# Optimization experiments

Hardware: AMD Instinct MI355X
Metric: run time of the kernel (lower is better)

Reference implementation:

```python
import jax, jax.numpy as jnp
import numpy as np

B, S, D = 4, 512, 2048      # batch, seq, hidden
DFF = 5632                   # SwiGLU intermediate
E, TOPK, R = 8, 2, 16        # experts, top-k, lora rank
SCALE = 32.0 / 16.0          # lora alpha / r


def setup_inputs() -> dict:
    key = jax.random.key(0)
    ks = jax.random.split(key, 18)
    rn = lambda k, shape, s=0.02: (jax.random.normal(k, shape, dtype=jnp.float32) * s)
    return {
        "data": jax.random.normal(ks[0], (B, S, D), dtype=jnp.float32),
        # shared base SwiGLU MLP (gate/up/down projections)
        "W1": rn(ks[1], (DFF, D)),
        "W3": rn(ks[2], (DFF, D)),
        "W2": rn(ks[3], (D, DFF)),
        # MixLoRA MoE adapter: router gate + per-expert LoRA on w1/w3/w2
        "gate_W": rn(ks[4], (E, D)),
        "A1": rn(ks[5], (E, R, D)), "B1": rn(ks[6], (E, DFF, R)),
        "A3": rn(ks[7], (E, R, D)), "B3": rn(ks[8], (E, DFF, R)),
        "A2": rn(ks[9], (E, R, DFF)), "B2": rn(ks[10], (E, D, R)),
        # plain LoRA adapter (second batch segment, _lora_forward path)
        "la1": rn(ks[11], (R, D)), "lb1": rn(ks[12], (DFF, R)),
        "la3": rn(ks[13], (R, D)), "lb3": rn(ks[14], (DFF, R)),
        "la2": rn(ks[15], (R, DFF)), "lb2": rn(ks[16], (D, R)),
    }


def reference(data, W1, W3, W2, gate_W, A1, B1, A3, B3, A2, B2,
              la1, lb1, la3, lb3, la2, lb2):
    half = B // 2

    # ---- segment 0: MixLoRA MoE adapter ----
    x = data[:half].reshape(-1, D)                      # [N, D] tokens
    N = x.shape[0]
    logits = x @ gate_W.T                               # [N, E] router logits
    probs = jax.nn.softmax(logits, axis=-1)
    topw, topi = jax.lax.top_k(probs, TOPK)
    topw = topw / jnp.sum(topw, axis=-1, keepdims=True)
    # dense routing weights (zero for non-selected experts)
    wd = jnp.zeros((N, E), x.dtype).at[jnp.arange(N)[:, None], topi].set(topw)

    bg = x @ W1.T                                       # [N, DFF] base gate proj
    bu = x @ W3.T                                       # [N, DFF] base up proj
    dg = jnp.einsum('enr,efr->enf', jnp.einsum('nd,erd->enr', x, A1), B1)
    du = jnp.einsum('enr,efr->enf', jnp.einsum('nd,erd->enr', x, A3), B3)
    h = jax.nn.silu(bg[None] + SCALE * dg) * (bu[None] + SCALE * du)  # [E,N,DFF]
    oe = jnp.einsum('enf,df->end', h, W2) \
        + SCALE * jnp.einsum('enr,edr->end', jnp.einsum('enf,erf->enr', h, A2), B2)
    moe_out = jnp.einsum('ne,end->nd', wd, oe).reshape(half, S, D)

    # ---- segment 1: plain LoRA adapter (_lora_forward) ----
    x2 = data[half:]                                    # [half, S, D]
    g2 = jax.nn.silu(x2 @ W1.T + SCALE * ((x2 @ la1.T) @ lb1.T))
    u2 = x2 @ W3.T + SCALE * ((x2 @ la3.T) @ lb3.T)
    h2 = g2 * u2
    out2 = h2 @ W2.T + SCALE * ((h2 @ la2.T) @ lb2.T)

    # index_copy over contiguous per-segment ranges == concat along dim 0
    final = jnp.concatenate([moe_out, out2], axis=0)    # [B, S, D]
    return final, logits
```

## Files before the change

kernel.cpp:

```cpp
#include <hip/hip_runtime.h>
#include <hip/hip_bf16.h>

#define DEVI __device__ __forceinline__

typedef __attribute__((ext_vector_type(8))) short short8;
typedef __attribute__((ext_vector_type(4))) float f32x4;

constexpr int D    = 2048;
constexpr int DFF  = 5632;
constexpr int NTOK = 2048;
constexpr int NMOE = 1024;
constexpr float KSCALE = 2.0f;

constexpr int NW      = 11648;
constexpr int COL_A1  = 11264;
constexpr int COL_A3  = 11392;
constexpr int COL_LA1 = 11520;
constexpr int COL_LA3 = 11536;

DEVI float bf2f(unsigned short u) { return __uint_as_float(((unsigned)u) << 16); }
DEVI unsigned short f2bf(float f) {
  unsigned u = __float_as_uint(f);
  u += 0x7FFFu + ((u >> 16) & 1u);
  return (unsigned short)(u >> 16);
}
DEVI float silu(float x) { return x / (1.f + __expf(-x)); }

struct CastSegs {
  const float* src[14];
  unsigned short* dst[14];
  int blk_end[14];
};

__global__ __launch_bounds__(256) void cast_segs_kernel(CastSegs cs) {
  int b = blockIdx.x;
  int s = 0;
  #pragma unroll
  for (int i = 0; i < 14; ++i) if (b >= cs.blk_end[i]) s = i + 1;
  int bstart = (s == 0) ? 0 : cs.blk_end[s - 1];
  size_t idx = ((size_t)(b - bstart) * 256 + threadIdx.x) * 4;
  float4 v = *(const float4*)(cs.src[s] + idx);
  ushort4 o;
  o.x = f2bf(v.x); o.y = f2bf(v.y); o.z = f2bf(v.z); o.w = f2bf(v.w);
  *(ushort4*)(cs.dst[s] + idx) = o;
}

__global__ __launch_bounds__(256) void transpose_ra_kernel(const float* __restrict__ A2,
                                                           const float* __restrict__ la2,
                                                           unsigned short* __restrict__ A2tb,
                                                           unsigned short* __restrict__ la2tb) {
  int f = blockIdx.x * 256 + threadIdx.x;
  int e = blockIdx.y;
  const float* src = (e < 8) ? (A2 + (size_t)e * 16 * DFF) : la2;
  unsigned short* dst = (e < 8) ? (A2tb + (size_t)e * DFF * 16) : la2tb;
  unsigned short tmp[16];
  #pragma unroll
  for (int r = 0; r < 16; ++r) tmp[r] = f2bf(src[(size_t)r * DFF + f]);
  #pragma unroll
  for (int r = 0; r < 16; ++r) dst[(size_t)f * 16 + r] = tmp[r];
}

__global__ __launch_bounds__(256) void gate_kernel(const float* __restrict__ x,
                                                   const float* __restrict__ gW,
                                                   float* __restrict__ logits_out,
                                                   int* __restrict__ gidx,
                                                   float* __restrict__ gwt) {
  int t = blockIdx.x * 4 + (threadIdx.x >> 6);
  int lane = threadIdx.x & 63;
  const float* xr = x + (size_t)t * D;
  float acc[8];
  #pragma unroll
  for (int e = 0; e < 8; ++e) acc[e] = 0.f;
  for (int k = lane; k < D; k += 64) {
    float xv = xr[k];
    #pragma unroll
    for (int e = 0; e < 8; ++e) acc[e] = fmaf(xv, gW[e * D + k], acc[e]);
  }
  #pragma unroll
  for (int e = 0; e < 8; ++e) {
    float v = acc[e];
    #pragma unroll
    for (int s = 32; s > 0; s >>= 1) v += __shfl_xor(v, s);
    acc[e] = v;
  }
  if (lane == 0) {
    #pragma unroll
    for (int e = 0; e < 8; ++e) logits_out[(size_t)t * 8 + e] = acc[e];
    int i1 = 0;
    #pragma unroll
    for (int e = 1; e < 8; ++e) if (acc[e] > acc[i1]) i1 = e;
    int i2 = (i1 == 0) ? 1 : 0;
    #pragma unroll
    for (int e = 0; e < 8; ++e) if (e != i1 && acc[e] > acc[i2]) i2 = e;
    float w1 = 1.f / (1.f + expf(acc[i2] - acc[i1]));
    gidx[t * 2] = i1; gidx[t * 2 + 1] = i2;
    gwt[t * 2] = w1;  gwt[t * 2 + 1] = 1.f - w1;
  }
}

typedef const void __attribute__((address_space(1)))* gp1_t;
typedef void __attribute__((address_space(3)))* lp3_t;
DEVI void gload_lds16(const void* g, void* l) {
  __builtin_amdgcn_global_load_lds((gp1_t)g, (lp3_t)l, 16, 0, 0);
}
#define S_BARRIER() asm volatile("s_barrier" ::: "memory")
#define LGKM0() do { asm volatile("s_waitcnt lgkmcnt(0)" ::: "memory"); \
                     __builtin_amdgcn_sched_barrier(0); } while (0)

template <int N> DEVI void vmcnt_() {
  static_assert(N == 0 || N == 4, "enumerate literals");
  if constexpr (N == 0)  asm volatile("s_waitcnt vmcnt(0)" ::: "memory");
  if constexpr (N == 4)  asm volatile("s_waitcnt vmcnt(4)" ::: "memory");
}

template <int BM, int BN, int WM, int WN, int MINW, int EPI>
__global__ __launch_bounds__(WM * WN * 64, MINW) void gemmP(
    const unsigned short* __restrict__ A,
    const unsigned short* __restrict__ B,
    int K,
    float* __restrict__ Cf,
    unsigned short* __restrict__ Cb,
    const float* __restrict__ addv,
    int ldc, int nbx) {
  constexpr int THREADS = WM * WN * 64;
  constexpr int RW = BM / WM;
  constexpr int CW = BN / WN;
  static_assert(RW == 64 && CW == 64, "template assumes 64x64 per-wave tile");
  constexpr int ATILE = BM * 128;
  constexpr int BTILE = BN * 128;
  constexpr int SLOT = ATILE + BTILE;
  constexpr int APARTS = BM * 8 / THREADS;
  constexpr int BPARTS = BN * 8 / THREADS;
  constexpr int BH = BPARTS / 2;

  __shared__ __align__(16) char smem[2 * SLOT];

  const int tid = threadIdx.x;
  const int wave = tid >> 6, lane = tid & 63;
  const int wm = wave / WN, wn = wave % WN;
  const int r15 = lane & 15, g = lane >> 4;

  const int nwg = (int)gridDim.x;
  const int bid = (int)blockIdx.x;
  const int wgid = (bid & 7) * (nwg >> 3) + (bid >> 3);
  const int bx = wgid % nbx, by = wgid / nbx;

  const unsigned short* Ablk = A + (size_t)by * BM * K;
  const unsigned short* Bblk = B + (size_t)bx * BN * K;

  int sgoA[APARTS], sgoB[BPARTS];
  #pragma unroll
  for (int j = 0; j < APARTS; ++j) {
    int tt = j * THREADS + tid;
    int row = tt >> 3;
    sgoA[j] = row * K + (((tt & 7) ^ (row & 7)) << 3);
  }
  #pragma unroll
  for (int j = 0; j < BPARTS; ++j) {
    int tt = j * THREADS + tid;
    int row = tt >> 3;
    sgoB[j] = row * K + (((tt & 7) ^ (row & 7)) << 3);
  }
  auto stageA = [&](int p, int k0) {
    char* s = smem + p * SLOT;
    #pragma unroll
    for (int j = 0; j < APARTS; ++j)
      gload_lds16((const char*)Ablk + ((size_t)(sgoA[j] + k0) << 1),
                  s + j * (THREADS * 16) + wave * 1024);
  };
  auto stageBh = [&](int p, int k0, int h) {
    char* s = smem + p * SLOT + ATILE;
    #pragma unroll
    for (int j = 0; j < BH; ++j)
      gload_lds16((const char*)Bblk + ((size_t)(sgoB[h * BH + j] + k0) << 1),
                  s + (h * BH + j) * (THREADS * 16) + wave * 1024);
  };

  const int arow0 = (wm * RW + r15) * 128;
  const int brow0 = (wn * CW + r15) * 128;
  const int s0 = ((g ^ (r15 & 7)) << 4);
  const int s1 = (((4 + g) ^ (r15 & 7)) << 4);

  f32x4 acc[4][4];
  #pragma unroll
  for (int m = 0; m < 4; ++m)
    #pragma unroll
    for (int n = 0; n < 4; ++n)
      #pragma unroll
      for (int j = 0; j < 4; ++j) acc[m][n][j] = 0.f;

  const int NT = K >> 6;

  stageA(0, 0);
  stageBh(0, 0, 0);
  stageBh(0, 0, 1);

  for (int t = 0; t < NT; ++t) {
    const int p = t & 1;
    const bool hn = (t + 1) < NT;
    const int k0n = (t + 1) << 6;
    if (hn) {
      stageA(p ^ 1, k0n);
      vmcnt_<4>();
    } else {
      vmcnt_<0>();
    }
    S_BARRIER();

    const char* sA = smem + p * SLOT;
    const char* sB = sA + ATILE;

    short8 bq[4][2], af[2][2];
    #pragma unroll
    for (int n = 0; n < 4; ++n) {
      bq[n][0] = *(const short8*)(sB + brow0 + n * 2048 + s0);
      bq[n][1] = *(const short8*)(sB + brow0 + n * 2048 + s1);
    }
    #pragma unroll
    for (int i = 0; i < 2; ++i) {
      af[i][0] = *(const short8*)(sA + arow0 + i * 2048 + s0);
      af[i][1] = *(const short8*)(sA + arow0 + i * 2048 + s1);
    }
    if (hn) stageBh(p ^ 1, k0n, 0);
    S_BARRIER();
    LGKM0();
    __builtin_amdgcn_s_setprio(1);
    #pragma unroll
    for (int i = 0; i < 2; ++i)
      #pragma unroll
      for (int n = 0; n < 4; ++n)
        #pragma unroll
        for (int kk = 0; kk < 2; ++kk)
          acc[i][n] = __builtin_amdgcn_mfma_f32_16x16x32_bf16(
              af[i][kk], bq[n][kk], acc[i][n], 0, 0, 0);
    __builtin_amdgcn_s_setprio(0);

    short8 ag[2][2];
    #pragma unroll
    for (int i = 0; i < 2; ++i) {
      ag[i][0] = *(const short8*)(sA + arow0 + (2 + i) * 2048 + s0);
      ag[i][1] = *(const short8*)(sA + arow0 + (2 + i) * 2048 + s1);
    }
    if (hn) stageBh(p ^ 1, k0n, 1);
    S_BARRIER();
    LGKM0();
    __builtin_amdgcn_s_setprio(1);
    #pragma unroll
    for (int i = 0; i < 2; ++i)
      #pragma unroll
      for (int n = 0; n < 4; ++n)
        #pragma unroll
        for (int kk = 0; kk < 2; ++kk)
          acc[2 + i][n] = __builtin_amdgcn_mfma_f32_16x16x32_bf16(
              ag[i][kk], bq[n][kk], acc[2 + i][n], 0, 0, 0);
    __builtin_amdgcn_s_setprio(0);

    S_BARRIER();
  }

  const int row0 = by * BM + wm * RW + (g << 2);
  const int col0 = bx * BN + wn * CW + r15;
  #pragma unroll
  for (int m = 0; m < 4; ++m) {
    #pragma unroll
    for (int n = 0; n < 4; ++n) {
      int col = col0 + n * 16;
      #pragma unroll
      for (int j = 0; j < 4; ++j) {
        int row = row0 + m * 16 + j;
        size_t off = (size_t)row * ldc + col;
        float v = acc[m][n][j];
        if (EPI == 1) Cb[off] = f2bf(v);
        else          Cf[off] = v + addv[off];
      }
    }
  }
}

DEVI float dot16bf(const float* a, const unsigned short* w) {
  short8 w0 = *(const short8*)w;
  short8 w1 = *(const short8*)(w + 8);
  float s = 0.f;
  #pragma unroll
  for (int i = 0; i < 8; ++i) s = fmaf(a[i],     bf2f((unsigned short)w0[i]), s);
  #pragma unroll
  for (int i = 0; i < 8; ++i) s = fmaf(a[8 + i], bf2f((unsigned short)w1[i]), s);
  return s;
}

__global__ __launch_bounds__(256) void h_kernel(
    const unsigned short* __restrict__ GU,
    const unsigned short* __restrict__ B1b,
    const unsigned short* __restrict__ B3b,
    const unsigned short* __restrict__ A2tb,
    const unsigned short* __restrict__ lb1b,
    const unsigned short* __restrict__ lb3b,
    const unsigned short* __restrict__ la2tb,
    const int* __restrict__ gidx, const float* __restrict__ gwt,
    unsigned short* __restrict__ Hb,
    float* __restrict__ qw) {
  const int t = blockIdx.x;
  const int tid = threadIdx.x;
  const unsigned short* gu = GU + (size_t)t * NW;
  unsigned short* hrow = Hb + (size_t)t * DFF;
  float qacc[32];
  #pragma unroll
  for (int r = 0; r < 32; ++r) qacc[r] = 0.f;
  float w1 = 0.f, w2 = 0.f;

  if (t < NMOE) {
    const int e1 = gidx[t * 2], e2 = gidx[t * 2 + 1];
    w1 = gwt[t * 2]; w2 = gwt[t * 2 + 1];
    float xa1a[16], xa1b[16], xa3a[16], xa3b[16];
    #pragma unroll
    for (int r = 0; r < 16; ++r) {
      xa1a[r] = bf2f(gu[COL_A1 + e1 * 16 + r]);
      xa1b[r] = bf2f(gu[COL_A1 + e2 * 16 + r]);
      xa3a[r] = bf2f(gu[COL_A3 + e1 * 16 + r]);
      xa3b[r] = bf2f(gu[COL_A3 + e2 * 16 + r]);
    }
    const unsigned short* B1e1 = B1b + (size_t)e1 * DFF * 16;
    const unsigned short* B1e2 = B1b + (size_t)e2 * DFF * 16;
    const unsigned short* B3e1 = B3b + (size_t)e1 * DFF * 16;
    const unsigned short* B3e2 = B3b + (size_t)e2 * DFF * 16;
    const unsigned short* A2e1 = A2tb + (size_t)e1 * DFF * 16;
    const unsigned short* A2e2 = A2tb + (size_t)e2 * DFF * 16;
    for (int i = 0; i < 22; ++i) {
      int f = tid + i * 256;
      float bg = bf2f(gu[f]), bu = bf2f(gu[DFF + f]);
      float dg1 = dot16bf(xa1a, B1e1 + f * 16);
      float du1 = dot16bf(xa3a, B3e1 + f * 16);
      float dg2 = dot16bf(xa1b, B1e2 + f * 16);
      float du2 = dot16bf(xa3b, B3e2 + f * 16);
      float h1 = silu(bg + KSCALE * dg1) * (bu + KSCALE * du1);
      float h2 = silu(bg + KSCALE * dg2) * (bu + KSCALE * du2);
      hrow[f] = f2bf(w1 * h1 + w2 * h2);
      short8 a0 = *(const short8*)(A2e1 + f * 16);
      short8 a1 = *(const short8*)(A2e1 + f * 16 + 8);
      short8 b0 = *(const short8*)(A2e2 + f * 16);
      short8 b1 = *(const short8*)(A2e2 + f * 16 + 8);
      #pragma unroll
      for (int r = 0; r < 8; ++r) {
        qacc[r]      = fmaf(h1, bf2f((unsigned short)a0[r]), qacc[r]);
        qacc[8 + r]  = fmaf(h1, bf2f((unsigned short)a1[r]), qacc[8 + r]);
        qacc[16 + r] = fmaf(h2, bf2f((unsigned short)b0[r]), qacc[16 + r]);
        qacc[24 + r] = fmaf(h2, bf2f((unsigned short)b1[r]), qacc[24 + r]);
      }
    }
  } else {
    float s1[16], s3[16];
    #pragma unroll
    for (int r = 0; r < 16; ++r) {
      s1[r] = bf2f(gu[COL_LA1 + r]);
      s3[r] = bf2f(gu[COL_LA3 + r]);
    }
    for (int i = 0; i < 22; ++i) {
      int f = tid + i * 256;
      float bg = bf2f(gu[f]), bu = bf2f(gu[DFF + f]);
      float dg = dot16bf(s1, lb1b + f * 16);
      float du = dot16bf(s3, lb3b + f * 16);
      float h = silu(bg + KSCALE * dg) * (bu + KSCALE * du);
      hrow[f] = f2bf(h);
      short8 a0 = *(const short8*)(la2tb + f * 16);
      short8 a1 = *(const short8*)(la2tb + f * 16 + 8);
      #pragma unroll
      for (int r = 0; r < 8; ++r) {
        qacc[r]     = fmaf(h, bf2f((unsigned short)a0[r]), qacc[r]);
        qacc[8 + r] = fmaf(h, bf2f((unsigned short)a1[r]), qacc[8 + r]);
      }
    }
  }

  #pragma unroll
  for (int r = 0; r < 32; ++r) {
    float v = qacc[r];
    #pragma unroll
    for (int s = 32; s > 0; s >>= 1) v += __shfl_xor(v, s);
    qacc[r] = v;
  }
  __shared__ float red[4][32];
  const int wave = tid >> 6, lane = tid & 63;
  if (lane == 0) {
    #pragma unroll
    for (int r = 0; r < 32; ++r) red[wave][r] = qacc[r];
  }
  __syncthreads();
  if (tid < 32) {
    float v = red[0][tid] + red[1][tid] + red[2][tid] + red[3][tid];
    float sc = (t < NMOE) ? ((tid < 16) ? (KSCALE * w1) : (KSCALE * w2)) : KSCALE;
    qw[(size_t)t * 32 + tid] = v * sc;
  }
}

__global__ __launch_bounds__(256) void ylora_kernel(const float* __restrict__ qw,
                                                    const unsigned short* __restrict__ B2b,
                                                    const unsigned short* __restrict__ lb2b,
                                                    const int* __restrict__ gidx,
                                                    float* __restrict__ ylora) {
  const int t = blockIdx.x;
  const int tid = threadIdx.x;
  const float* qr = qw + (size_t)t * 32;
  float q1[16], q2[16];
  #pragma unroll
  for (int r = 0; r < 16; ++r) { q1[r] = qr[r]; q2[r] = qr[16 + r]; }
  if (t < NMOE) {
    const unsigned short* p1 = B2b + (size_t)gidx[t * 2] * D * 16;
    const unsigned short* p2 = B2b + (size_t)gidx[t * 2 + 1] * D * 16;
    #pragma unroll
    for (int i = 0; i < 8; ++i) {
      int d = tid + i * 256;
      ylora[(size_t)t * D + d] = dot16bf(q1, p1 + d * 16) + dot16bf(q2, p2 + d * 16);
    }
  } else {
    #pragma unroll
    for (int i = 0; i < 8; ++i) {
      int d = tid + i * 256;
      ylora[(size_t)t * D + d] = dot16bf(q1, lb2b + d * 16);
    }
  }
}

extern "C" void kernel_launch(void* const* d_in, const int* in_sizes, int n_in,
                              void* d_out, int out_size, void* d_ws, size_t ws_size,
                              hipStream_t stream) {
  (void)in_sizes; (void)n_in; (void)out_size; (void)ws_size;
  const float* data = (const float*)d_in[0];
  const float* W1   = (const float*)d_in[1];
  const float* W3   = (const float*)d_in[2];
  const float* W2   = (const float*)d_in[3];
  const float* gW   = (const float*)d_in[4];
  const float* A1   = (const float*)d_in[5];
  const float* B1   = (const float*)d_in[6];
  const float* A3   = (const float*)d_in[7];
  const float* B3   = (const float*)d_in[8];
  const float* A2   = (const float*)d_in[9];
  const float* B2   = (const float*)d_in[10];
  const float* la1  = (const float*)d_in[11];
  const float* lb1  = (const float*)d_in[12];
  const float* la3  = (const float*)d_in[13];
  const float* lb3  = (const float*)d_in[14];
  const float* la2  = (const float*)d_in[15];
  const float* lb2  = (const float*)d_in[16];

  char* w = (char*)d_ws;
  size_t off = 0;
  auto alloc = [&](size_t bytes) -> char* {
    char* p = w + off;
    off += (bytes + 255) & ~(size_t)255;
    return p;
  };
  unsigned short* xb    = (unsigned short*)alloc((size_t)NTOK * D * 2);
  unsigned short* W13b  = (unsigned short*)alloc((size_t)NW * D * 2);
  unsigned short* W2b   = (unsigned short*)alloc((size_t)D * DFF * 2);
  unsigned short* B1b   = (unsigned short*)alloc((size_t)8 * DFF * 16 * 2);
  unsigned short* B3b   = (unsigned short*)alloc((size_t)8 * DFF * 16 * 2);
  unsigned short* A2tb  = (unsigned short*)alloc((size_t)8 * DFF * 16 * 2);
  unsigned short* la2tb = (unsigned short*)alloc((size_t)DFF * 16 * 2);
  unsigned short* lb1b  = (unsigned short*)alloc((size_t)DFF * 16 * 2);
  unsigned short* lb3b  = (unsigned short*)alloc((size_t)DFF * 16 * 2);
  unsigned short* lb2b  = (unsigned short*)alloc((size_t)D * 16 * 2);
  unsigned short* B2b   = (unsigned short*)alloc((size_t)8 * D * 16 * 2);
  int*   gidx = (int*)alloc((size_t)NMOE * 2 * 4);
  float* gwt  = (float*)alloc((size_t)NMOE * 2 * 4);
  unsigned short* GU    = (unsigned short*)alloc((size_t)NTOK * NW * 2);

  unsigned short* Hb = W13b;
  float* ylora = (float*)((char*)W13b + (size_t)NTOK * DFF * 2);
  float* qw    = (float*)xb;

  CastSegs cs;
  const float* srcs[14] = {data, W1, W3, W2, A1, A3, la1, la3, B1, B3, lb1, lb3, lb2, B2};
  unsigned short* dsts[14] = {
      xb, W13b, W13b + (size_t)DFF * D, W2b,
      W13b + (size_t)COL_A1 * D, W13b + (size_t)COL_A3 * D,
      W13b + (size_t)COL_LA1 * D, W13b + (size_t)COL_LA3 * D,
      B1b, B3b, lb1b, lb3b, lb2b, B2b};
  int ns[14] = {NTOK * D, DFF * D, DFF * D, DFF * D, 128 * D, 128 * D, 16 * D, 16 * D,
                8 * DFF * 16, 8 * DFF * 16, DFF * 16, DFF * 16, D * 16, 8 * D * 16};
  int total_blocks = 0;
  for (int i = 0; i < 14; ++i) {
    cs.src[i] = srcs[i];
    cs.dst[i] = dsts[i];
    total_blocks += ns[i] / 1024;
    cs.blk_end[i] = total_blocks;
  }
  cast_segs_kernel<<<total_blocks, 256, 0, stream>>>(cs);
  transpose_ra_kernel<<<dim3(DFF / 256, 9), 256, 0, stream>>>(A2, la2, A2tb, la2tb);
  hipMemsetAsync(W13b + (size_t)11552 * D, 0, (size_t)(NW - 11552) * D * 2, stream);

  gate_kernel<<<NMOE / 4, 256, 0, stream>>>(data, gW,
      (float*)d_out + (size_t)NTOK * D, gidx, gwt);

  gemmP<256, 128, 4, 2, 2, 1><<<(NTOK / 256) * (NW / 128), 512, 0, stream>>>(
      xb, W13b, D, (float*)nullptr, GU, (const float*)nullptr, NW, NW / 128);

  h_kernel<<<NTOK, 256, 0, stream>>>(GU, B1b, B3b, A2tb, lb1b, lb3b, la2tb,
                                     gidx, gwt, Hb, qw);

  ylora_kernel<<<NTOK, 256, 0, stream>>>(qw, B2b, lb2b, gidx, ylora);

  gemmP<128, 128, 2, 2, 2, 2><<<(NTOK / 128) * (D / 128), 256, 0, stream>>>(
      Hb, W2b, DFF, (float*)d_out, (unsigned short*)nullptr, ylora, D, D / 128);
}
```

Measured before the change: 358.1 us.

## Simplify GEMM pipeline to single-stage prefetch and shrink gate/up tile

The split-phase GEMM schedule is removed. It used to stage B in two halves between partial MFMA blocks, with extra barriers, lgkmcnt waits and setprio hints. Now each K-tile loads A and B in one prefetch, waits with vmcnt(8), reads all fragments, then runs the full 4x4 MFMA block. The gate/up projection GEMM also moves from 256x128 tiles with 8 waves to 128x128 tiles with 4 waves, doubling the grid. The aim is fewer barriers and better occupancy or load balance, at the cost of less interleaving of loads with compute and more redundant B-tile traffic.

```diff
diff --git a/kernel.cpp b/kernel.cpp
--- a/kernel.cpp
+++ b/kernel.cpp
@@ -104,17 +104,15 @@
   __builtin_amdgcn_global_load_lds((gp1_t)g, (lp3_t)l, 16, 0, 0);
 }
 #define S_BARRIER() asm volatile("s_barrier" ::: "memory")
-#define LGKM0() do { asm volatile("s_waitcnt lgkmcnt(0)" ::: "memory"); \
-                     __builtin_amdgcn_sched_barrier(0); } while (0)
 
 template <int N> DEVI void vmcnt_() {
-  static_assert(N == 0 || N == 4, "enumerate literals");
-  if constexpr (N == 0)  asm volatile("s_waitcnt vmcnt(0)" ::: "memory");
-  if constexpr (N == 4)  asm volatile("s_waitcnt vmcnt(4)" ::: "memory");
+  static_assert(N == 0 || N == 8, "enumerate literals");
+  if constexpr (N == 0) asm volatile("s_waitcnt vmcnt(0)" ::: "memory");
+  if constexpr (N == 8) asm volatile("s_waitcnt vmcnt(8)" ::: "memory");
 }
 
 template <int BM, int BN, int WM, int WN, int MINW, int EPI>
-__global__ __launch_bounds__(WM * WN * 64, MINW) void gemmP(
+__global__ __launch_bounds__(WM * WN * 64, MINW) void gemmM(
     const unsigned short* __restrict__ A,
     const unsigned short* __restrict__ B,
     int K,
@@ -131,7 +129,7 @@
   constexpr int SLOT = ATILE + BTILE;
   constexpr int APARTS = BM * 8 / THREADS;
   constexpr int BPARTS = BN * 8 / THREADS;
-  constexpr int BH = BPARTS / 2;
+  static_assert(APARTS + BPARTS == 8, "vmcnt gate literal assumes 8 loads/tile");
 
   __shared__ __align__(16) char smem[2 * SLOT];
 
@@ -161,19 +159,16 @@
     int row = tt >> 3;
     sgoB[j] = row * K + (((tt & 7) ^ (row & 7)) << 3);
   }
-  auto stageA = [&](int p, int k0) {
+  auto stage = [&](int p, int k0) {
     char* s = smem + p * SLOT;
     #pragma unroll
     for (int j = 0; j < APARTS; ++j)
       gload_lds16((const char*)Ablk + ((size_t)(sgoA[j] + k0) << 1),
                   s + j * (THREADS * 16) + wave * 1024);
-  };
-  auto stageBh = [&](int p, int k0, int h) {
-    char* s = smem + p * SLOT + ATILE;
-    #pragma unroll
-    for (int j = 0; j < BH; ++j)
-      gload_lds16((const char*)Bblk + ((size_t)(sgoB[h * BH + j] + k0) << 1),
-                  s + (h * BH + j) * (THREADS * 16) + wave * 1024);
+    #pragma unroll
+    for (int j = 0; j < BPARTS; ++j)
+      gload_lds16((const char*)Bblk + ((size_t)(sgoB[j] + k0) << 1),
+                  s + ATILE + j * (THREADS * 16) + wave * 1024);
   };
 
   const int arow0 = (wm * RW + r15) * 128;
@@ -191,17 +186,13 @@
 
   const int NT = K >> 6;
 
-  stageA(0, 0);
-  stageBh(0, 0, 0);
-  stageBh(0, 0, 1);
+  stage(0, 0);
 
   for (int t = 0; t < NT; ++t) {
     const int p = t & 1;
-    const bool hn = (t + 1) < NT;
-    const int k0n = (t + 1) << 6;
-    if (hn) {
-      stageA(p ^ 1, k0n);
-      vmcnt_<4>();
+    if (t + 1 < NT) {
+      stage(p ^ 1, (t + 1) << 6);
+      vmcnt_<8>();
     } else {
       vmcnt_<0>();
     }
@@ -210,50 +201,25 @@
     const char* sA = smem + p * SLOT;
     const char* sB = sA + ATILE;
 
-    short8 bq[4][2], af[2][2];
+    short8 bq[4][2], av[4][2];
     #pragma unroll
     for (int n = 0; n < 4; ++n) {
       bq[n][0] = *(const short8*)(sB + brow0 + n * 2048 + s0);
       bq[n][1] = *(const short8*)(sB + brow0 + n * 2048 + s1);
     }
     #pragma unroll
-    for (int i = 0; i < 2; ++i) {
-      af[i][0] = *(const short8*)(sA + arow0 + i * 2048 + s0);
-      af[i][1] = *(const short8*)(sA + arow0 + i * 2048 + s1);
-    }
-    if (hn) stageBh(p ^ 1, k0n, 0);
-    S_BARRIER();
-    LGKM0();
-    __builtin_amdgcn_s_setprio(1);
-    #pragma unroll
-    for (int i = 0; i < 2; ++i)
+    for (int m = 0; m < 4; ++m) {
+      av[m][0] = *(const short8*)(sA + arow0 + m * 2048 + s0);
+      av[m][1] = *(const short8*)(sA + arow0 + m * 2048 + s1);
+    }
+    #pragma unroll
+    for (int m = 0; m < 4; ++m)
       #pragma unroll
       for (int n = 0; n < 4; ++n)
         #pragma unroll
         for (int kk = 0; kk < 2; ++kk)
-          acc[i][n] = __builtin_amdgcn_mfma_f32_16x16x32_bf16(
-              af[i][kk], bq[n][kk], acc[i][n], 0, 0, 0);
-    __builtin_amdgcn_s_setprio(0);
-
-    short8 ag[2][2];
-    #pragma unroll
-    for (int i = 0; i < 2; ++i) {
-      ag[i][0] = *(const short8*)(sA + arow0 + (2 + i) * 2048 + s0);
-      ag[i][1] = *(const short8*)(sA + arow0 + (2 + i) * 2048 + s1);
-    }
-    if (hn) stageBh(p ^ 1, k0n, 1);
-    S_BARRIER();
-    LGKM0();
-    __builtin_amdgcn_s_setprio(1);
-    #pragma unroll
-    for (int i = 0; i < 2; ++i)
-      #pragma unroll
-      for (int n = 0; n < 4; ++n)
-        #pragma unroll
-        for (int kk = 0; kk < 2; ++kk)
-          acc[2 + i][n] = __builtin_amdgcn_mfma_f32_16x16x32_bf16(
-              ag[i][kk], bq[n][kk], acc[2 + i][n], 0, 0, 0);
-    __builtin_amdgcn_s_setprio(0);
+          acc[m][n] = __builtin_amdgcn_mfma_f32_16x16x32_bf16(
+              av[m][kk], bq[n][kk], acc[m][n], 0, 0, 0);
 
     S_BARRIER();
   }
@@ -491,7 +457,7 @@
   gate_kernel<<<NMOE / 4, 256, 0, stream>>>(data, gW,
       (float*)d_out + (size_t)NTOK * D, gidx, gwt);
 
-  gemmP<256, 128, 4, 2, 2, 1><<<(NTOK / 256) * (NW / 128), 512, 0, stream>>>(
+  gemmM<128, 128, 2, 2, 2, 1><<<(NTOK / 128) * (NW / 128), 256, 0, stream>>>(
       xb, W13b, D, (float*)nullptr, GU, (const float*)nullptr, NW, NW / 128);
 
   h_kernel<<<NTOK, 256, 0, stream>>>(GU, B1b, B3b, A2tb, lb1b, lb3b, la2tb,
@@ -499,6 +465,6 @@
 
   ylora_kernel<<<NTOK, 256, 0, stream>>>(qw, B2b, lb2b, gidx, ylora);
 
-  gemmP<128, 128, 2, 2, 2, 2><<<(NTOK / 128) * (D / 128), 256, 0, stream>>>(
+  gemmM<128, 128, 2, 2, 2, 2><<<(NTOK / 128) * (D / 128), 256, 0, stream>>>(
       Hb, W2b, DFF, (float*)d_out, (unsigned short*)nullptr, ylora, D, D / 128);
 }
```

New measurement: 351.7 us. About the same (-1.8%).
